# Kernel tuning notes

Hardware: AMD Instinct MI355X
Metric: run time of the kernel (lower is better)

Reference implementation:

```python
import jax, jax.numpy as jnp
import numpy as np

B, NP, C_IN, H = 8, 6250, 512, 256   # graphs, nodes/graph, in-feat, hidden
EPG = 100000                          # edges per graph
K = 5000                              # ceil(0.8 * NP) kept by TopKPooling
H3 = 3 * H


def setup_inputs() -> dict:
    key = jax.random.key(0)
    ks = jax.random.split(key, 16)
    N, E = B * NP, B * EPG
    x = jax.random.normal(ks[0], (N, C_IN), jnp.float32)
    offs = (jnp.arange(E) // EPG) * NP  # keep edges inside their graph
    src = jax.random.randint(ks[1], (E,), 0, NP) + offs
    dst = jax.random.randint(ks[2], (E,), 0, NP) + offs
    edge_index = jnp.stack([src, dst]).astype(jnp.int64)
    edge_attr = jax.random.uniform(ks[3], (E,), jnp.float32)
    batch = jnp.repeat(jnp.arange(B), NP).astype(jnp.int64)
    s = 0.05
    W1 = jax.random.normal(ks[4], (C_IN, H), jnp.float32) * s
    b1 = jnp.zeros((H,), jnp.float32)
    W2 = jax.random.normal(ks[5], (H, H), jnp.float32) * s
    b2 = jnp.zeros((H,), jnp.float32)
    pw = jax.random.normal(ks[6], (H3,), jnp.float32) * s   # TopKPooling attn vector
    lw1 = jax.random.normal(ks[7], (H3 * 2, H), jnp.float32) * s
    lb1 = jnp.zeros((H,), jnp.float32)
    lw2 = jax.random.normal(ks[8], (H, H // 2), jnp.float32) * s
    lb2 = jnp.zeros((H // 2,), jnp.float32)
    lw3 = jax.random.normal(ks[9], (H // 2, 3), jnp.float32) * s
    lb3 = jnp.zeros((3,), jnp.float32)
    return {"x": x, "edge_index": edge_index, "edge_attr": edge_attr, "batch": batch,
            "W1": W1, "b1": b1, "W2": W2, "b2": b2, "pw": pw,
            "lw1": lw1, "lb1": lb1, "lw2": lw2, "lb2": lb2, "lw3": lw3, "lb3": lb3}


def _gcn(x, W, b, src, dst, ew, n):
    xw = x @ W
    deg = jnp.zeros((n,), xw.dtype).at[dst].add(ew) + 1.0
    dinv = jax.lax.rsqrt(deg)
    norm = dinv[src] * ew * dinv[dst]
    out = jnp.zeros_like(xw).at[dst].add(norm[:, None] * xw[src])
    return out + (dinv * dinv)[:, None] * xw + b


def reference(x, edge_index, edge_attr, batch, W1, b1, W2, b2, pw,
              lw1, lb1, lw2, lb2, lw3, lb3):
    N = x.shape[0]
    src, dst = edge_index[0], edge_index[1]
    x1 = jax.nn.relu(_gcn(x, W1, b1, src, dst, edge_attr, N))
    x2 = jax.nn.relu(_gcn(x1, W2, b2, src, dst, edge_attr, N))
    x3 = jax.nn.relu(_gcn(x2, W2, b2, src, dst, edge_attr, N))  # conv2 reused (as in source)
    cat_x = jnp.concatenate([x1, x2, x3], axis=1)               # [N, 3H]
    # TopKPooling: score = sigmoid((x . w) / ||w||), keep top-K per graph, scale by score
    score = jax.nn.sigmoid((cat_x @ pw) / jnp.linalg.norm(pw))   # [N]
    sc = score.reshape(B, NP)
    topv, topi = jax.lax.top_k(sc, K)                            # [B, K]
    xg = cat_x.reshape(B, NP, H3)
    sel = jnp.take_along_axis(xg, topi[:, :, None], axis=1) * topv[:, :, None]  # [B, K, 3H]
    readout = jnp.concatenate([sel.mean(axis=1), sel.max(axis=1)], axis=1)      # [B, 6H]
    h = jax.nn.relu(readout @ lw1 + lb1)
    h = jax.nn.relu(h @ lw2 + lb2)       # dropout p=0 is a no-op
    return h @ lw3 + lb3                 # [B, 3]
```

## Files before the change

### kernel.cpp

```cpp
#include <hip/hip_runtime.h>
#include <stdint.h>

#define NODES  50000
#define MPAD   50048
#define NGRAPH 8
#define NP_G   6250
#define EDGES  800000
#define KKEEP  5000
#define HID    256
#define CIN    512
#define H3     768
#define SCANB  196
#define RCHUNK 200
#define MLPCH  24
#define MLPCK  64

#define K1_EDGE  3125
#define K1_CAST  25000
#define K1_W1    512
#define K1_W2    256
#define K1_TOTAL (K1_EDGE + K1_CAST + K1_W1 + K1_W2 + 1)
#define K2_GEMM  782
#define K2_TOTAL (K2_GEMM + 3125)

using f32x4  = __attribute__((ext_vector_type(4))) float;
using bf16x8 = __attribute__((ext_vector_type(8))) short;
using u16x8  = __attribute__((ext_vector_type(8))) unsigned short;
typedef unsigned short u16;
typedef unsigned long long u64;

__device__ __forceinline__ float bf2f(u16 u) {
    return __uint_as_float(((uint32_t)u) << 16);
}
__device__ __forceinline__ u16 f2bf(float f) {
    uint32_t u = __float_as_uint(f);
    u += 0x7fffu + ((u >> 16) & 1u);
    return (u16)(u >> 16);
}

__global__ __launch_bounds__(256) void k1_kernel(
        const int* __restrict__ ei, const float* __restrict__ ew,
        u64* __restrict__ degcnt,
        const float* __restrict__ x, u16* __restrict__ A0,
        const float* __restrict__ W1, const float* __restrict__ W2,
        const float* __restrict__ pw,
        u16* __restrict__ Wt1, u16* __restrict__ Wt2, float* __restrict__ invn) {
    __shared__ float sh[256];
    int b = blockIdx.x, t = threadIdx.x;
    if (b < K1_EDGE) {
        int e = b * 256 + t;
        int d = ei[EDGES + e];
        u64 enc = (1ull << 48) | (u64)(ew[e] * 4294967296.0f);
        atomicAdd(&degcnt[d], enc);
    } else if (b < K1_EDGE + K1_CAST) {
        size_t base = ((size_t)(b - K1_EDGE) * 256 + t) * 4;
        float4 v = *(const float4*)(x + base);
        ushort4 o;
        o.x = f2bf(v.x); o.y = f2bf(v.y); o.z = f2bf(v.z); o.w = f2bf(v.w);
        *(ushort4*)(A0 + base) = o;
    } else if (b < K1_EDGE + K1_CAST + K1_W1) {
        int id = (b - K1_EDGE - K1_CAST) * 256 + t;
        int n = id >> 9, k = id & 511;
        Wt1[id] = f2bf(W1[(size_t)k * HID + n]);
    } else if (b < K1_TOTAL - 1) {
        int id = (b - K1_EDGE - K1_CAST - K1_W1) * 256 + t;
        int n = id >> 8, k = id & 255;
        Wt2[id] = f2bf(W2[(size_t)k * HID + n]);
    } else {
        float s = 0.f;
        for (int i = t; i < H3; i += 256) { float v = pw[i]; s += v * v; }
        sh[t] = s; __syncthreads();
        for (int off = 128; off; off >>= 1) {
            if (t < off) sh[t] += sh[t + off];
            __syncthreads();
        }
        if (t == 0) invn[0] = rsqrtf(sh[0]);
    }
}

__global__ void scan1_kernel(const u64* __restrict__ degcnt,
                             int* __restrict__ iscan, int* __restrict__ bsum,
                             float* __restrict__ dinv) {
    int b = blockIdx.x, t = threadIdx.x;
    int i = b * 256 + t;
    int c = 0;
    if (i < NODES) {
        u64 dc = degcnt[i];
        c = (int)(dc >> 48);
        float deg = (float)(dc & 0xFFFFFFFFFFFFull) * (1.0f / 4294967296.0f);
        dinv[i] = rsqrtf(deg + 1.0f);
    }
    int lane = t & 63, wv = t >> 6;
    int v = c;
    for (int off = 1; off < 64; off <<= 1) {
        int u = __shfl_up(v, off);
        if (lane >= off) v += u;
    }
    __shared__ int ws[4];
    if (lane == 63) ws[wv] = v;
    __syncthreads();
    if (t == 0) { int s = 0; for (int k = 0; k < 4; k++) { int tmp = ws[k]; ws[k] = s; s += tmp; } }
    __syncthreads();
    v += ws[wv];
    if (i < NODES) iscan[i] = v;
    if (t == 255) bsum[b] = v;
}

__global__ void scan2_kernel(const int* __restrict__ bsum, int* __restrict__ boff) {
    int t = threadIdx.x;
    int c = (t < SCANB) ? bsum[t] : 0;
    int lane = t & 63, wv = t >> 6;
    int v = c;
    for (int off = 1; off < 64; off <<= 1) {
        int u = __shfl_up(v, off);
        if (lane >= off) v += u;
    }
    __shared__ int ws[4];
    if (lane == 63) ws[wv] = v;
    __syncthreads();
    if (t == 0) { int s = 0; for (int k = 0; k < 4; k++) { int tmp = ws[k]; ws[k] = s; s += tmp; } }
    __syncthreads();
    v += ws[wv];
    if (t < SCANB) boff[t] = v - c;
}

__global__ void scan3_kernel(const u64* __restrict__ degcnt,
                             const int* __restrict__ iscan, const int* __restrict__ boff,
                             int* __restrict__ rowptr, int* __restrict__ rowcur) {
    int b = blockIdx.x, t = threadIdx.x;
    int i = b * 256 + t;
    if (i > NODES) return;
    if (i == NODES) { rowptr[NODES] = EDGES; return; }
    int c = (int)(degcnt[i] >> 48);
    int v = boff[b] + iscan[i] - c;
    rowptr[i] = v;
    rowcur[i] = v;
}

__device__ __forceinline__ void gemm_body(const u16* __restrict__ A,
                                          const u16* __restrict__ Bt,
                                          u16* __restrict__ C,
                                          int K, int bm, int bn,
                                          u16* As, u16* Bs) {
    const int tid  = threadIdx.x;
    const int wave = tid >> 6, lane = tid & 63;
    const int wm = wave >> 1, wn = wave & 1;
    const int quad = lane >> 4, l16 = lane & 15;
    const int sr = tid >> 2;
    const int sc = tid & 3;
    const int swz = (sc ^ ((sr >> 1) & 3)) * 8;
    const int rphys = (quad ^ ((l16 >> 1) & 3)) * 8;

    const u16* Ag = A + (size_t)(bm * 128 + sr) * K + sc * 8;
    const u16* Bg = Bt + (size_t)(bn * 128 + sr) * K + sc * 8;

    f32x4 acc[4][4];
#pragma unroll
    for (int i = 0; i < 4; i++)
#pragma unroll
        for (int j = 0; j < 4; j++) { f32x4 z = {0.f, 0.f, 0.f, 0.f}; acc[i][j] = z; }

    for (int k0 = 0; k0 < K; k0 += 32) {
        int4 av0 = *(const int4*)(Ag + k0);
        int4 av1 = *(const int4*)(Ag + (size_t)64 * K + k0);
        int4 bv0 = *(const int4*)(Bg + k0);
        int4 bv1 = *(const int4*)(Bg + (size_t)64 * K + k0);
        __syncthreads();
        *(int4*)(As + sr * 32 + swz)        = av0;
        *(int4*)(As + (sr + 64) * 32 + swz) = av1;
        *(int4*)(Bs + sr * 32 + swz)        = bv0;
        *(int4*)(Bs + (sr + 64) * 32 + swz) = bv1;
        __syncthreads();
        bf16x8 af[4], bfr[4];
#pragma unroll
        for (int i = 0; i < 4; i++)
            af[i] = *(const bf16x8*)(As + (wm * 64 + i * 16 + l16) * 32 + rphys);
#pragma unroll
        for (int j = 0; j < 4; j++)
            bfr[j] = *(const bf16x8*)(Bs + (wn * 64 + j * 16 + l16) * 32 + rphys);
#pragma unroll
        for (int i = 0; i < 4; i++)
#pragma unroll
            for (int j = 0; j < 4; j++)
                acc[i][j] = __builtin_amdgcn_mfma_f32_16x16x32_bf16(af[i], bfr[j], acc[i][j], 0, 0, 0);
    }

    const int crow0 = bm * 128 + wm * 64 + quad * 4;
    const int ccol0 = bn * 128 + wn * 64 + l16;
#pragma unroll
    for (int i = 0; i < 4; i++)
#pragma unroll
        for (int j = 0; j < 4; j++)
#pragma unroll
            for (int r = 0; r < 4; r++)
                C[(size_t)(crow0 + i * 16 + r) * HID + ccol0 + j * 16] = f2bf(acc[i][j][r]);
}

__global__ __launch_bounds__(256) void k2_kernel(
        const u16* __restrict__ A0, const u16* __restrict__ Wt1, u16* __restrict__ xw,
        const int* __restrict__ ei, const float* __restrict__ ew,
        const float* __restrict__ dinv,
        int* __restrict__ rowcur, int2* __restrict__ csr) {
    __shared__ u16 As[128 * 32];
    __shared__ u16 Bs[128 * 32];
    int b = blockIdx.x;
    if (b < K2_GEMM) {
        gemm_body(A0, Wt1, xw, CIN, b >> 1, b & 1, As, Bs);
    } else {
        int e = (b - K2_GEMM) * 256 + threadIdx.x;
        int s = ei[e], d = ei[EDGES + e];
        int pos = atomicAdd(&rowcur[d], 1);
        csr[pos] = make_int2(s, __float_as_int(dinv[s] * ew[e] * dinv[d]));
    }
}

__global__ __launch_bounds__(256) void gemm_bt(const u16* __restrict__ A,
                                               const u16* __restrict__ Bt,
                                               u16* __restrict__ C, int K) {
    __shared__ u16 As[128 * 32];
    __shared__ u16 Bs[128 * 32];
    gemm_body(A, Bt, C, K, blockIdx.x, blockIdx.y, As, Bs);
}

template<bool SCORE>
__global__ void agg_kernel(const u16* __restrict__ xw, u16* __restrict__ xo,
                           const int* __restrict__ rowptr, const int2* __restrict__ csr,
                           const float* __restrict__ dinv, const float* __restrict__ bias,
                           const u16* __restrict__ xs1, const u16* __restrict__ xs2,
                           const float* __restrict__ pw, const float* __restrict__ invn,
                           float* __restrict__ score, u64* __restrict__ keys) {
    int wave = threadIdx.x >> 6;
    int lane = threadIdx.x & 63;
    int g  = blockIdx.x & 7;
    int nl = (blockIdx.x >> 3) * 4 + wave;
    if (nl >= NP_G) return;
    int w = g * NP_G + nl;
    int half = lane >> 5;
    int f8 = (lane & 31) * 8;
    size_t ro = (size_t)w * HID + f8;

    float accA[8], accB[8];
#pragma unroll
    for (int j = 0; j < 8; ++j) { accA[j] = 0.f; accB[j] = 0.f; }

    int p = rowptr[w], p1 = rowptr[w + 1];
    for (; p + 4 <= p1; p += 4) {
        int2 eA = csr[p + half];
        int2 eB = csr[p + 2 + half];
        float wA = __int_as_float(eA.y), wB = __int_as_float(eB.y);
        u16x8 vA = *(const u16x8*)(xw + (size_t)eA.x * HID + f8);
        u16x8 vB = *(const u16x8*)(xw + (size_t)eB.x * HID + f8);
#pragma unroll
        for (int j = 0; j < 8; ++j) {
            accA[j] += wA * bf2f(vA[j]);
            accB[j] += wB * bf2f(vB[j]);
        }
    }
    for (; p < p1; p += 2) {
        int idx = p + half;
        bool valid = idx < p1;
        int2 eA = csr[valid ? idx : p];
        float wA = valid ? __int_as_float(eA.y) : 0.f;
        u16x8 vA = *(const u16x8*)(xw + (size_t)eA.x * HID + f8);
#pragma unroll
        for (int j = 0; j < 8; ++j) accA[j] += wA * bf2f(vA[j]);
    }

#pragma unroll
    for (int j = 0; j < 8; ++j) {
        accA[j] += accB[j];
        accA[j] += __shfl(accA[j], lane ^ 32, 64);
    }

    float di = dinv[w], sw = di * di;
    u16x8 sv = *(const u16x8*)(xw + ro);
    float bb[8];
    {
        float4 t0 = *(const float4*)(bias + f8);
        float4 t1 = *(const float4*)(bias + f8 + 4);
        bb[0] = t0.x; bb[1] = t0.y; bb[2] = t0.z; bb[3] = t0.w;
        bb[4] = t1.x; bb[5] = t1.y; bb[6] = t1.z; bb[7] = t1.w;
    }
    u16x8 o;
    float ov[8];
#pragma unroll
    for (int j = 0; j < 8; ++j) {
        float v = fmaxf(accA[j] + sw * bf2f(sv[j]) + bb[j], 0.f);
        o[j] = f2bf(v);
        ov[j] = bf2f(o[j]);
    }
    if (half == 0) *(u16x8*)(xo + ro) = o;

    if (SCORE) {
        u16x8 v1 = *(const u16x8*)(xs1 + ro);
        u16x8 v2 = *(const u16x8*)(xs2 + ro);
        float acc = 0.f;
#pragma unroll
        for (int j = 0; j < 8; ++j) {
            acc += bf2f(v1[j]) * pw[f8 + j];
            acc += bf2f(v2[j]) * pw[256 + f8 + j];
            acc += ov[j]       * pw[512 + f8 + j];
        }
#pragma unroll
        for (int off = 1; off < 32; off <<= 1) acc += __shfl_xor(acc, off, 64);
        if (lane == 0) {
            float s = acc * invn[0];
            float sc = 1.f / (1.f + __expf(-s));
            score[w] = sc;
            keys[w] = ((u64)__float_as_uint(sc) << 13) | (unsigned int)(NP_G - 1 - nl);
        }
    }
}

__global__ __launch_bounds__(1024) void selcomp_kernel(
        const u64* __restrict__ keys, const float* __restrict__ score,
        int* __restrict__ selidx, float* __restrict__ selscr) {
    __shared__ u64 kk[NP_G];
    __shared__ unsigned int hist[4][256];
    __shared__ unsigned int sfx[257];
    __shared__ u64 spref;
    __shared__ unsigned int swant;
    int g = blockIdx.x, t = threadIdx.x;
    const u64* kg = keys + (size_t)g * NP_G;
    for (int i = t; i < NP_G; i += 1024) kk[i] = kg[i];
    if (t == 0) { spref = 0ull; swant = KKEEP; }
    const int wgrp = (t >> 8) & 3;
    u64 mask = 0ull;
    __syncthreads();
    for (int shift = 40; shift >= 0; shift -= 8) {
        if (t < 256) { hist[0][t] = 0; hist[1][t] = 0; hist[2][t] = 0; hist[3][t] = 0; }
        __syncthreads();
        u64 pref = spref;
        for (int i = t; i < NP_G; i += 1024) {
            u64 key = kk[i];
            if ((key & mask) == pref)
                atomicAdd(&hist[wgrp][(unsigned int)(key >> shift) & 255u], 1u);
        }
        __syncthreads();
        if (t < 256) sfx[t] = hist[0][t] + hist[1][t] + hist[2][t] + hist[3][t];
        if (t == 0) sfx[256] = 0;
        __syncthreads();
        for (int off = 1; off < 256; off <<= 1) {
            unsigned int v = 0;
            if (t < 256 && t + off < 256) v = sfx[t + off];
            __syncthreads();
            if (t < 256 && t + off < 256) sfx[t] += v;
            __syncthreads();
        }
        unsigned int want = swant;
        __syncthreads();
        if (t < 256) {
            unsigned int s0 = sfx[t], s1 = sfx[t + 1];
            if (s0 >= want && s1 < want) {
                spref = pref | ((u64)t << shift);
                swant = want - s1;
            }
        }
        __syncthreads();
        mask |= (255ull << shift);
    }
    u64 kth = spref;
    int lane = t & 63, wv = t >> 6;
    __shared__ int wsum[16];
    __shared__ int cbase;
    if (t == 0) cbase = 0;
    __syncthreads();
    for (int k = 0; k < (NP_G + 1023) / 1024; ++k) {
        int i = k * 1024 + t;
        bool sel = (i < NP_G) && (kk[i] >= kth);
        int n = g * NP_G + i;
        u64 bal = __ballot(sel);
        int prefix = __popcll(bal & ((1ull << lane) - 1ull));
        if (lane == 0) wsum[wv] = __popcll(bal);
        __syncthreads();
        if (t == 0) {
            int s = cbase;
            for (int j = 0; j < 16; ++j) { int tmp = wsum[j]; wsum[j] = s; s += tmp; }
            cbase = s;
        }
        __syncthreads();
        if (sel) {
            int pos = wsum[wv] + prefix;
            selidx[g * KKEEP + pos] = n;
            selscr[g * KKEEP + pos] = score[n];
        }
        __syncthreads();
    }
}

__global__ __launch_bounds__(256) void readout_kernel(
        const u16* __restrict__ x1, const u16* __restrict__ x2,
        const u16* __restrict__ x3,
        const int* __restrict__ selidx, const float* __restrict__ selscr,
        float* __restrict__ sumbuf, int* __restrict__ maxbuf) {
    int g = blockIdx.x, tpart = blockIdx.y, c = blockIdx.z;
    int fcol = threadIdx.x;
    const u16* xt = (tpart == 0) ? x1 : ((tpart == 1) ? x2 : x3);
    __shared__ int   sidx[RCHUNK];
    __shared__ float sscr[RCHUNK];
    int base = g * KKEEP + c * RCHUNK;
    if (fcol < RCHUNK) { sidx[fcol] = selidx[base + fcol]; sscr[fcol] = selscr[base + fcol]; }
    __syncthreads();
    float sum = 0.f, mx = 0.f;
#pragma unroll 1
    for (int j = 0; j < RCHUNK; j += 4) {
        int n0 = sidx[j], n1 = sidx[j + 1], n2 = sidx[j + 2], n3 = sidx[j + 3];
        float s0 = sscr[j], s1 = sscr[j + 1], s2 = sscr[j + 2], s3 = sscr[j + 3];
        float v0 = bf2f(xt[(size_t)n0 * HID + fcol]) * s0;
        float v1 = bf2f(xt[(size_t)n1 * HID + fcol]) * s1;
        float v2 = bf2f(xt[(size_t)n2 * HID + fcol]) * s2;
        float v3 = bf2f(xt[(size_t)n3 * HID + fcol]) * s3;
        sum += v0 + v1 + v2 + v3;
        mx = fmaxf(mx, fmaxf(fmaxf(v0, v1), fmaxf(v2, v3)));
    }
    int o = (g * 3 + tpart) * HID + fcol;
    atomicAdd(&sumbuf[o], sum);
    atomicMax(&maxbuf[o], __float_as_int(mx));
}

__global__ __launch_bounds__(256) void mlp1_kernel(const float* __restrict__ sumbuf,
                                                   const int* __restrict__ maxbuf,
                                                   const float* __restrict__ lw1,
                                                   float* __restrict__ h1acc) {
    int g = blockIdx.x, ch = blockIdx.y, t = threadIdx.x;
    __shared__ float r[MLPCK];
    int k0 = ch * MLPCK;
    if (t < MLPCK) {
        int i = k0 + t;
        r[t] = (i < 768) ? sumbuf[g * 768 + i] * (1.f / 5000.f)
                         : __int_as_float(maxbuf[g * 768 + (i - 768)]);
    }
    __syncthreads();
    float a0 = 0.f, a1 = 0.f, a2 = 0.f, a3 = 0.f;
#pragma unroll
    for (int i = 0; i < MLPCK; i += 4) {
        a0 += r[i]     * lw1[(size_t)(k0 + i)     * 256 + t];
        a1 += r[i + 1] * lw1[(size_t)(k0 + i + 1) * 256 + t];
        a2 += r[i + 2] * lw1[(size_t)(k0 + i + 2) * 256 + t];
        a3 += r[i + 3] * lw1[(size_t)(k0 + i + 3) * 256 + t];
    }
    atomicAdd(&h1acc[g * 256 + t], (a0 + a1) + (a2 + a3));
}

__global__ __launch_bounds__(256) void mlp2_kernel(const float* __restrict__ h1acc,
                                                   const float* __restrict__ lb1,
                                                   const float* __restrict__ lw2,
                                                   const float* __restrict__ lb2,
                                                   const float* __restrict__ lw3,
                                                   const float* __restrict__ lb3,
                                                   float* __restrict__ out) {
    __shared__ float h1[256];
    __shared__ float part[256];
    __shared__ float h2[128];
    int g = blockIdx.x, t = threadIdx.x;
    h1[t] = fmaxf(h1acc[g * 256 + t] + lb1[t], 0.f);
    __syncthreads();
    int col = t & 127, half = t >> 7;
    float a = 0.f;
#pragma unroll
    for (int i = 0; i < 128; i += 4) {
        int k = half * 128 + i;
        a += h1[k]     * lw2[k * 128 + col]
           + h1[k + 1] * lw2[(k + 1) * 128 + col]
           + h1[k + 2] * lw2[(k + 2) * 128 + col]
           + h1[k + 3] * lw2[(k + 3) * 128 + col];
    }
    part[t] = a;
    __syncthreads();
    if (t < 128) h2[t] = fmaxf(part[t] + part[t + 128] + lb2[t], 0.f);
    __syncthreads();
    if (t < 3) {
        float a3 = lb3[t];
        for (int i = 0; i < 128; ++i) a3 += h2[i] * lw3[i * 3 + t];
        out[g * 3 + t] = a3;
    }
}

extern "C" void kernel_launch(void* const* d_in, const int* in_sizes, int n_in,
                              void* d_out, int out_size, void* d_ws, size_t ws_size,
                              hipStream_t stream) {
    const float* x   = (const float*)d_in[0];
    const int*   ei  = (const int*)d_in[1];
    const float* ew  = (const float*)d_in[2];
    const float* W1  = (const float*)d_in[4];
    const float* b1  = (const float*)d_in[5];
    const float* W2  = (const float*)d_in[6];
    const float* b2  = (const float*)d_in[7];
    const float* pw  = (const float*)d_in[8];
    const float* lw1 = (const float*)d_in[9];
    const float* lb1 = (const float*)d_in[10];
    const float* lw2 = (const float*)d_in[11];
    const float* lb2 = (const float*)d_in[12];
    const float* lw3 = (const float*)d_in[13];
    const float* lb3 = (const float*)d_in[14];
    float* out = (float*)d_out;

    char* p = (char*)d_ws;
    auto alloc = [&](size_t bytes) -> char* {
        char* r = p;
        p += (bytes + 255) & ~(size_t)255;
        return r;
    };
    u16* A0  = (u16*)alloc((size_t)MPAD * CIN * 2);
    u16* x3  = (u16*)alloc((size_t)MPAD * HID * 2);
    u16* xw  = (u16*)alloc((size_t)MPAD * HID * 2);
    u16* Wt1 = (u16*)alloc((size_t)HID * CIN * 2);
    u16* Wt2 = (u16*)alloc((size_t)HID * HID * 2);
    int2*  csr    = (int2*)alloc((size_t)EDGES * 8);
    int*   rowptr = (int*)alloc((size_t)(NODES + 1) * 4);
    int*   rowcur = (int*)alloc((size_t)NODES * 4);
    int*   iscan  = (int*)alloc((size_t)NODES * 4);
    int*   bsum   = (int*)alloc((size_t)SCANB * 4);
    int*   boff   = (int*)alloc((size_t)SCANB * 4);
    u64*   keys   = (u64*)alloc((size_t)NODES * 8);
    float* score  = (float*)alloc((size_t)NODES * 4);
    float* dinv   = (float*)alloc((size_t)NODES * 4);
    int*   selidx = (int*)alloc((size_t)NGRAPH * KKEEP * 4);
    float* selscr = (float*)alloc((size_t)NGRAPH * KKEEP * 4);
    float* invn   = (float*)alloc(256);
    char* zbase = p;
    u64*   degcnt = (u64*)alloc((size_t)NODES * 8);
    float* sumbuf = (float*)alloc(6144 * 4);
    int*   maxbuf = (int*)alloc(6144 * 4);
    float* h1acc  = (float*)alloc((size_t)NGRAPH * 256 * 4);
    size_t zbytes = (size_t)(p - zbase);

    u16* x1 = A0;
    u16* x2 = A0 + (size_t)MPAD * HID;

    hipMemsetAsync(zbase, 0, zbytes, stream);

    k1_kernel<<<K1_TOTAL, 256, 0, stream>>>(ei, ew, degcnt, x, A0,
                                            W1, W2, pw, Wt1, Wt2, invn);
    scan1_kernel<<<SCANB, 256, 0, stream>>>(degcnt, iscan, bsum, dinv);
    scan2_kernel<<<1, 256, 0, stream>>>(bsum, boff);
    scan3_kernel<<<SCANB + 1, 256, 0, stream>>>(degcnt, iscan, boff, rowptr, rowcur);
    k2_kernel<<<K2_TOTAL, 256, 0, stream>>>(A0, Wt1, xw, ei, ew, dinv, rowcur, csr);

    dim3 gg(MPAD / 128, HID / 128);
    int aggBlocks = 8 * ((NP_G + 3) / 4);

    agg_kernel<false><<<aggBlocks, 256, 0, stream>>>(xw, x1, rowptr, csr, dinv, b1,
                                                     nullptr, nullptr, nullptr, nullptr,
                                                     nullptr, nullptr);
    gemm_bt<<<gg, 256, 0, stream>>>(x1, Wt2, xw, HID);
    agg_kernel<false><<<aggBlocks, 256, 0, stream>>>(xw, x2, rowptr, csr, dinv, b2,
                                                     nullptr, nullptr, nullptr, nullptr,
                                                     nullptr, nullptr);
    gemm_bt<<<gg, 256, 0, stream>>>(x2, Wt2, xw, HID);
    agg_kernel<true><<<aggBlocks, 256, 0, stream>>>(xw, x3, rowptr, csr, dinv, b2,
                                                    x1, x2, pw, invn, score, keys);

    selcomp_kernel<<<NGRAPH, 1024, 0, stream>>>(keys, score, selidx, selscr);
    readout_kernel<<<dim3(NGRAPH, 3, KKEEP / RCHUNK), 256, 0, stream>>>(
        x1, x2, x3, selidx, selscr, sumbuf, maxbuf);
    mlp1_kernel<<<dim3(NGRAPH, MLPCH), 256, 0, stream>>>(sumbuf, maxbuf, lw1, h1acc);
    mlp2_kernel<<<NGRAPH, 256, 0, stream>>>(h1acc, lb1, lw2, lb2, lw3, lb3, out);
}
```

Before: 520.8 us.

## Build degree histogram and CSR via per-block shared-memory partials instead of global atomics

Degree counting now splits each graph's edges into 32 slices. Each slice builds a shared-memory histogram over half the graph's nodes and writes it to a partial array. scan1 sums the 32 partials per node and stores an exclusive per-slice base, so the CSR fill can keep its cursors in LDS and use shared-memory atomics instead of global rowcur atomics. This is meant to remove contended global 64-bit and 32-bit atomics, at the cost of about 19 MB of extra partial/blockbase traffic and reading every edge twice in the histogram. It also assumes edges are stored contiguously per graph with in-graph destinations: out-of-range destinations are dropped from the degree count and could index outside the LDS cursor array during the fill.

```diff
diff --git a/kernel.cpp b/kernel.cpp
--- a/kernel.cpp
+++ b/kernel.cpp
@@ -5,6 +5,7 @@
 #define MPAD   50048
 #define NGRAPH 8
 #define NP_G   6250
+#define EPG    100000
 #define EDGES  800000
 #define KKEEP  5000
 #define HID    256
@@ -14,19 +15,22 @@
 #define RCHUNK 200
 #define MLPCH  24
 #define MLPCK  64
-
-#define K1_EDGE  3125
+#define ESL    3125
+
+#define K1_HIST  512
 #define K1_CAST  25000
 #define K1_W1    512
 #define K1_W2    256
-#define K1_TOTAL (K1_EDGE + K1_CAST + K1_W1 + K1_W2 + 1)
+#define K1_TOTAL (K1_HIST + K1_CAST + K1_W1 + K1_W2 + 1)
 #define K2_GEMM  782
-#define K2_TOTAL (K2_GEMM + 3125)
+#define K2_FILL  256
+#define K2_TOTAL (K2_GEMM + K2_FILL)
 
 using f32x4  = __attribute__((ext_vector_type(4))) float;
 using bf16x8 = __attribute__((ext_vector_type(8))) short;
 using u16x8  = __attribute__((ext_vector_type(8))) unsigned short;
 typedef unsigned short u16;
+typedef unsigned int   u32;
 typedef unsigned long long u64;
 
 __device__ __forceinline__ float bf2f(u16 u) {
@@ -40,33 +44,51 @@
 
 __global__ __launch_bounds__(256) void k1_kernel(
         const int* __restrict__ ei, const float* __restrict__ ew,
-        u64* __restrict__ degcnt,
+        u64* __restrict__ partial,
         const float* __restrict__ x, u16* __restrict__ A0,
         const float* __restrict__ W1, const float* __restrict__ W2,
         const float* __restrict__ pw,
         u16* __restrict__ Wt1, u16* __restrict__ Wt2, float* __restrict__ invn) {
-    __shared__ float sh[256];
+    __shared__ __align__(16) char smem[ESL * 8];
     int b = blockIdx.x, t = threadIdx.x;
-    if (b < K1_EDGE) {
-        int e = b * 256 + t;
-        int d = ei[EDGES + e];
-        u64 enc = (1ull << 48) | (u64)(ew[e] * 4294967296.0f);
-        atomicAdd(&degcnt[d], enc);
-    } else if (b < K1_EDGE + K1_CAST) {
-        size_t base = ((size_t)(b - K1_EDGE) * 256 + t) * 4;
+    if (b < K1_HIST) {
+        u64* hl = (u64*)smem;
+        int g  = b >> 6;
+        int r  = b & 63;
+        int bb = r >> 1;
+        int h  = r & 1;
+        for (int k = t; k < ESL; k += 256) hl[k] = 0ull;
+        __syncthreads();
+        int ebase = g * EPG + bb * ESL;
+        int lo = h * ESL;
+        for (int k = t; k < ESL; k += 256) {
+            int e = ebase + k;
+            int d = ei[EDGES + e];
+            int il = d - g * NP_G - lo;
+            if ((unsigned)il < (unsigned)ESL) {
+                u64 enc = (1ull << 48) | (u64)(ew[e] * 4294967296.0f);
+                atomicAdd(&hl[il], enc);
+            }
+        }
+        __syncthreads();
+        u64* prow = partial + (size_t)(g * 32 + bb) * NP_G + lo;
+        for (int k = t; k < ESL; k += 256) prow[k] = hl[k];
+    } else if (b < K1_HIST + K1_CAST) {
+        size_t base = ((size_t)(b - K1_HIST) * 256 + t) * 4;
         float4 v = *(const float4*)(x + base);
         ushort4 o;
         o.x = f2bf(v.x); o.y = f2bf(v.y); o.z = f2bf(v.z); o.w = f2bf(v.w);
         *(ushort4*)(A0 + base) = o;
-    } else if (b < K1_EDGE + K1_CAST + K1_W1) {
-        int id = (b - K1_EDGE - K1_CAST) * 256 + t;
+    } else if (b < K1_HIST + K1_CAST + K1_W1) {
+        int id = (b - K1_HIST - K1_CAST) * 256 + t;
         int n = id >> 9, k = id & 511;
         Wt1[id] = f2bf(W1[(size_t)k * HID + n]);
     } else if (b < K1_TOTAL - 1) {
-        int id = (b - K1_EDGE - K1_CAST - K1_W1) * 256 + t;
+        int id = (b - K1_HIST - K1_CAST - K1_W1) * 256 + t;
         int n = id >> 8, k = id & 255;
         Wt2[id] = f2bf(W2[(size_t)k * HID + n]);
     } else {
+        float* sh = (float*)smem;
         float s = 0.f;
         for (int i = t; i < H3; i += 256) { float v = pw[i]; s += v * v; }
         sh[t] = s; __syncthreads();
@@ -78,16 +100,27 @@
     }
 }
 
-__global__ void scan1_kernel(const u64* __restrict__ degcnt,
+__global__ void scan1_kernel(const u64* __restrict__ partial,
+                             u32* __restrict__ blockbase,
                              int* __restrict__ iscan, int* __restrict__ bsum,
                              float* __restrict__ dinv) {
     int b = blockIdx.x, t = threadIdx.x;
     int i = b * 256 + t;
     int c = 0;
     if (i < NODES) {
-        u64 dc = degcnt[i];
-        c = (int)(dc >> 48);
-        float deg = (float)(dc & 0xFFFFFFFFFFFFull) * (1.0f / 4294967296.0f);
+        int g = i / NP_G, il = i - g * NP_G;
+        size_t base = (size_t)(g * 32) * NP_G + il;
+        u64 fix = 0ull; u32 cnt = 0;
+#pragma unroll 4
+        for (int j = 0; j < 32; ++j) {
+            size_t idx = base + (size_t)j * NP_G;
+            u64 pv = partial[idx];
+            blockbase[idx] = cnt;
+            cnt += (u32)(pv >> 48);
+            fix += pv & 0xFFFFFFFFFFFFull;
+        }
+        c = (int)cnt;
+        float deg = (float)fix * (1.0f / 4294967296.0f);
         dinv[i] = rsqrtf(deg + 1.0f);
     }
     int lane = t & 63, wv = t >> 6;
@@ -102,7 +135,7 @@
     if (t == 0) { int s = 0; for (int k = 0; k < 4; k++) { int tmp = ws[k]; ws[k] = s; s += tmp; } }
     __syncthreads();
     v += ws[wv];
-    if (i < NODES) iscan[i] = v;
+    if (i < NODES) iscan[i] = v - c;
     if (t == 255) bsum[b] = v;
 }
 
@@ -124,17 +157,13 @@
     if (t < SCANB) boff[t] = v - c;
 }
 
-__global__ void scan3_kernel(const u64* __restrict__ degcnt,
-                             const int* __restrict__ iscan, const int* __restrict__ boff,
-                             int* __restrict__ rowptr, int* __restrict__ rowcur) {
+__global__ void scan3_kernel(const int* __restrict__ iscan, const int* __restrict__ boff,
+                             int* __restrict__ rowptr) {
     int b = blockIdx.x, t = threadIdx.x;
     int i = b * 256 + t;
     if (i > NODES) return;
     if (i == NODES) { rowptr[NODES] = EDGES; return; }
-    int c = (int)(degcnt[i] >> 48);
-    int v = boff[b] + iscan[i] - c;
-    rowptr[i] = v;
-    rowcur[i] = v;
+    rowptr[i] = boff[b] + iscan[i];
 }
 
 __device__ __forceinline__ void gemm_body(const u16* __restrict__ A,
@@ -199,18 +228,31 @@
 __global__ __launch_bounds__(256) void k2_kernel(
         const u16* __restrict__ A0, const u16* __restrict__ Wt1, u16* __restrict__ xw,
         const int* __restrict__ ei, const float* __restrict__ ew,
-        const float* __restrict__ dinv,
-        int* __restrict__ rowcur, int2* __restrict__ csr) {
-    __shared__ u16 As[128 * 32];
-    __shared__ u16 Bs[128 * 32];
+        const float* __restrict__ dinv, const int* __restrict__ rowptr,
+        const u32* __restrict__ blockbase, int2* __restrict__ csr) {
+    __shared__ __align__(16) char smem[NP_G * 4];
     int b = blockIdx.x;
     if (b < K2_GEMM) {
+        u16* As = (u16*)smem;
+        u16* Bs = (u16*)(smem + 8192);
         gemm_body(A0, Wt1, xw, CIN, b >> 1, b & 1, As, Bs);
     } else {
-        int e = (b - K2_GEMM) * 256 + threadIdx.x;
-        int s = ei[e], d = ei[EDGES + e];
-        int pos = atomicAdd(&rowcur[d], 1);
-        csr[pos] = make_int2(s, __float_as_int(dinv[s] * ew[e] * dinv[d]));
+        u32* cursor = (u32*)smem;
+        int fb = b - K2_GEMM;
+        int g = fb >> 5, bb = fb & 31;
+        const u32* bbase = blockbase + (size_t)(g * 32 + bb) * NP_G;
+        const int* rp = rowptr + g * NP_G;
+        for (int k = threadIdx.x; k < NP_G; k += 256)
+            cursor[k] = (u32)rp[k] + bbase[k];
+        __syncthreads();
+        int ebase = g * EPG + bb * ESL;
+        for (int k = threadIdx.x; k < ESL; k += 256) {
+            int e = ebase + k;
+            int s = ei[e], d = ei[EDGES + e];
+            int il = d - g * NP_G;
+            u32 pos = atomicAdd(&cursor[il], 1u);
+            csr[pos] = make_int2(s, __float_as_int(dinv[s] * ew[e] * dinv[d]));
+        }
     }
 }
 
@@ -507,8 +549,9 @@
     u16* Wt1 = (u16*)alloc((size_t)HID * CIN * 2);
     u16* Wt2 = (u16*)alloc((size_t)HID * HID * 2);
     int2*  csr    = (int2*)alloc((size_t)EDGES * 8);
+    u64*   partial   = (u64*)alloc((size_t)256 * NP_G * 8);
+    u32*   blockbase = (u32*)alloc((size_t)256 * NP_G * 4);
     int*   rowptr = (int*)alloc((size_t)(NODES + 1) * 4);
-    int*   rowcur = (int*)alloc((size_t)NODES * 4);
     int*   iscan  = (int*)alloc((size_t)NODES * 4);
     int*   bsum   = (int*)alloc((size_t)SCANB * 4);
     int*   boff   = (int*)alloc((size_t)SCANB * 4);
@@ -519,7 +562,6 @@
     float* selscr = (float*)alloc((size_t)NGRAPH * KKEEP * 4);
     float* invn   = (float*)alloc(256);
     char* zbase = p;
-    u64*   degcnt = (u64*)alloc((size_t)NODES * 8);
     float* sumbuf = (float*)alloc(6144 * 4);
     int*   maxbuf = (int*)alloc(6144 * 4);
     float* h1acc  = (float*)alloc((size_t)NGRAPH * 256 * 4);
@@ -530,12 +572,13 @@
 
     hipMemsetAsync(zbase, 0, zbytes, stream);
 
-    k1_kernel<<<K1_TOTAL, 256, 0, stream>>>(ei, ew, degcnt, x, A0,
+    k1_kernel<<<K1_TOTAL, 256, 0, stream>>>(ei, ew, partial, x, A0,
                                             W1, W2, pw, Wt1, Wt2, invn);
-    scan1_kernel<<<SCANB, 256, 0, stream>>>(degcnt, iscan, bsum, dinv);
+    scan1_kernel<<<SCANB, 256, 0, stream>>>(partial, blockbase, iscan, bsum, dinv);
     scan2_kernel<<<1, 256, 0, stream>>>(bsum, boff);
-    scan3_kernel<<<SCANB + 1, 256, 0, stream>>>(degcnt, iscan, boff, rowptr, rowcur);
-    k2_kernel<<<K2_TOTAL, 256, 0, stream>>>(A0, Wt1, xw, ei, ew, dinv, rowcur, csr);
+    scan3_kernel<<<SCANB + 1, 256, 0, stream>>>(iscan, boff, rowptr);
+    k2_kernel<<<K2_TOTAL, 256, 0, stream>>>(A0, Wt1, xw, ei, ew, dinv, rowptr,
+                                            blockbase, csr);
 
     dim3 gg(MPAD / 128, HID / 128);
     int aggBlocks = 8 * ((NP_G + 3) / 4);
```

After: 488.9 us. -6.1%, faster.
